# Performance work log

Measured on AMD Instinct MI355X. Metric: run time of the kernel, lower is better.

The kernel has to match this reference:

```python
import jax, jax.numpy as jnp
import numpy as np
import math

NUM_HEADS = 8
EPS = 1e-5
LEAKY_SLOPE = 0.01


def _attention(q, k, v, mask):
    # q:[S,64] k,v:[T,64] -> [S,64]; scale by sqrt(d) per source (q.shape[1])
    s = (q @ k.T) / math.sqrt(q.shape[1])
    if mask:
        S, T = s.shape
        tri = jnp.tril(jnp.ones((S, T), dtype=bool))
        s = jnp.where(tri, s, -jnp.inf)
    return jax.nn.softmax(s, axis=1) @ v


def _mha(q, k, v, w_o, mask):
    # all heads share the same (q,k,v) in the source, so cat over heads == tile
    head = _attention(q, k, v, mask)            # [S,64]
    concat = jnp.tile(head, (1, NUM_HEADS))     # [S,512]
    return concat @ w_o


def _layernorm(x, g, b):
    mu = jnp.mean(x, axis=-1, keepdims=True)
    var = jnp.var(x, axis=-1, keepdims=True)
    return (x - mu) * jax.lax.rsqrt(var + EPS) * g + b


def setup_inputs() -> dict:
    key = jax.random.key(0)
    ks = jax.random.split(key, 12)
    S, D, P, H = 8192, 512, 64, 2048
    sd = 1.0 / math.sqrt(D)
    return {
        "encoder_output": jax.random.normal(ks[0], (S, D), jnp.float32),
        "previous_stage_output": jax.random.normal(ks[1], (S, D), jnp.float32),
        "wq_m": jax.random.normal(ks[2], (D, P), jnp.float32) * sd,
        "wk_m": jax.random.normal(ks[3], (D, P), jnp.float32) * sd,
        "wv_m": jax.random.normal(ks[4], (D, P), jnp.float32) * sd,
        "wq_c": jax.random.normal(ks[5], (D, P), jnp.float32) * sd,
        "wk_c": jax.random.normal(ks[6], (D, P), jnp.float32) * sd,
        "wv_c": jax.random.normal(ks[7], (D, P), jnp.float32) * sd,
        "w_o": jax.random.normal(ks[8], (D, D), jnp.float32) * sd,
        "ln_g": jnp.ones((D,), jnp.float32),
        "ln_b": jnp.zeros((D,), jnp.float32),
        "w1": jax.random.normal(ks[9], (D, H), jnp.float32) * sd,
        "b1": jnp.zeros((H,), jnp.float32),
        "w2": jax.random.normal(ks[10], (H, D), jnp.float32) * (1.0 / math.sqrt(H)),
        "b2": jnp.zeros((D,), jnp.float32),
    }


def reference(encoder_output, previous_stage_output, wq_m, wk_m, wv_m,
              wq_c, wk_c, wv_c, w_o, ln_g, ln_b, w1, b1, w2, b2):
    prev = previous_stage_output
    # masked (causal) self-attention over previous decoder output
    masked_mh = _mha(prev @ wq_m, prev @ wk_m, prev @ wv_m, w_o, mask=True)
    # cross attention: q from masked output, k/v from encoder output
    mh = _mha(masked_mh @ wq_c, encoder_output @ wk_c, encoder_output @ wv_c,
              w_o, mask=False)
    x = _layernorm(mh + prev, ln_g, ln_b)
    h = x @ w1 + b1
    h = jnp.where(h >= 0, h, LEAKY_SLOPE * h)
    ffn = h @ w2 + b2
    out = _layernorm(ffn + x, ln_g, ln_b)
    return (encoder_output, out)
```

## Files before the change

kernel.cpp:

```cpp
#include <hip/hip_runtime.h>
#include <hip/hip_bf16.h>

typedef unsigned short u16;
typedef __attribute__((ext_vector_type(4))) float f32x4;
typedef __attribute__((ext_vector_type(8))) __bf16 bf16x8;
typedef __attribute__((ext_vector_type(8))) short short8;
typedef __attribute__((ext_vector_type(4))) short s16x4;

constexpr int SEQ = 8192;
constexpr int DM  = 512;
constexpr int HD  = 64;
constexpr int HFF = 2048;

__device__ __forceinline__ float b2f(u16 u){
  union { unsigned int i; float f; } v; v.i = ((unsigned int)u) << 16; return v.f;
}
__device__ __forceinline__ u16 f2b(float f){
  union { float f; unsigned int i; } v; v.f = f;
  unsigned int r = v.i + 0x7FFFu + ((v.i >> 16) & 1u);
  return (u16)(r >> 16);
}

__device__ __forceinline__ void gload16(const u16* g, u16* lds){
  __builtin_amdgcn_global_load_lds(
      (const __attribute__((address_space(1))) void*)g,
      (__attribute__((address_space(3))) void*)lds, 16, 0, 0);
}

__global__ __launch_bounds__(256) void cvt2_k(const float* __restrict__ enc,
                                              const float* __restrict__ prev,
                                              float* __restrict__ outf,
                                              u16* __restrict__ enc_b,
                                              u16* __restrict__ prev_b, long n8){
  long i = blockIdx.x * 256L + threadIdx.x;
  if(i >= n8) return;
  const float* in = blockIdx.y ? prev : enc;
  u16* ob = blockIdx.y ? prev_b : enc_b;
  f32x4 a = ((const f32x4*)in)[i*2];
  f32x4 b = ((const f32x4*)in)[i*2+1];
  if(!blockIdx.y){
    ((f32x4*)outf)[i*2]   = a;
    ((f32x4*)outf)[i*2+1] = b;
  }
  u16 ov[8];
  for(int j=0;j<4;j++){ ov[j] = f2b(a[j]); ov[4+j] = f2b(b[j]); }
  ((short8*)ob)[i] = *(short8*)ov;
}

__global__ __launch_bounds__(256) void prep_k(const float* __restrict__ p0,
                                              const float* __restrict__ p1,
                                              const float* __restrict__ p2,
                                              const float* __restrict__ p3,
                                              const float* __restrict__ p4,
                                              const float* __restrict__ p5,
                                              const float* __restrict__ w1,
                                              const float* __restrict__ w2,
                                              const float* __restrict__ wo,
                                              u16* __restrict__ out6,
                                              u16* __restrict__ w1_t,
                                              u16* __restrict__ w2_t,
                                              u16* __restrict__ wost,
                                              u16* __restrict__ wop){
  __shared__ u16 t[32][33];
  const int z = blockIdx.z;
  const int tx = threadIdx.x, ty = threadIdx.y;
  if(z < 6){
    if(blockIdx.x >= 2) return;
    const float* ins[6] = {p0,p1,p2,p3,p4,p5};
    const float* in = ins[z];
    u16* o = out6 + (long)z * 32768;
    int c0 = blockIdx.x*32, r0 = blockIdx.y*32;
    for(int i=0;i<4;i++)
      t[ty+i*8][tx] = f2b(in[(long)(r0+ty+i*8)*HD + c0+tx]);
    __syncthreads();
    for(int i=0;i<4;i++) o[(long)(c0+ty+i*8)*DM + r0+tx] = t[tx][ty+i*8];
  } else if(z == 6){
    int c0 = blockIdx.x*32, r0 = blockIdx.y*32;
    for(int i=0;i<4;i++)
      t[ty+i*8][tx] = f2b(w1[(long)(r0+ty+i*8)*HFF + c0+tx]);
    __syncthreads();
    for(int i=0;i<4;i++) w1_t[(long)(c0+ty+i*8)*DM + r0+tx] = t[tx][ty+i*8];
  } else if(z == 7){
    int c0 = blockIdx.y*32, r0 = blockIdx.x*32;
    for(int i=0;i<4;i++)
      t[ty+i*8][tx] = f2b(w2[(long)(r0+ty+i*8)*DM + c0+tx]);
    __syncthreads();
    for(int i=0;i<4;i++) w2_t[(long)(c0+ty+i*8)*HFF + r0+tx] = t[tx][ty+i*8];
  } else {
    int fb = blockIdx.y*64 + blockIdx.x;
    if(fb >= 128) return;
    int tid = fb*256 + ty*32 + tx;
    int n = tid >> 6, p = tid & 63;
    float s = 0.f;
    for(int h=0; h<8; h++) s += wo[(long)(h*64+p)*DM + n];
    u16 sv = f2b(s);
    wost[n*64 + p]  = sv;
    wop[p*DM + n]   = sv;
  }
}

__global__ __launch_bounds__(256) void vtrans2_k(const u16* __restrict__ v0,
                                                 u16* __restrict__ o0,
                                                 const u16* __restrict__ v1,
                                                 u16* __restrict__ o1){
  __shared__ u16 t[32][33];
  const u16* in = blockIdx.z ? v1 : v0;
  u16* o = blockIdx.z ? o1 : o0;
  int c0 = blockIdx.x*32, r0 = blockIdx.y*32;
  int tx = threadIdx.x, ty = threadIdx.y;
  for(int i=0;i<4;i++) t[ty+i*8][tx] = in[(long)(r0+ty+i*8)*HD + c0+tx];
  __syncthreads();
  for(int i=0;i<4;i++) o[(long)(c0+ty+i*8)*SEQ + r0+tx] = t[tx][ty+i*8];
}

template<bool WRITE_BF>
__global__ __launch_bounds__(256) void add_ln(const u16* __restrict__ Xa,
                                              const float* __restrict__ Xb,
                                              const float* __restrict__ G,
                                              const float* __restrict__ Bb,
                                              float* __restrict__ OutF,
                                              u16* __restrict__ OutB){
  int row  = blockIdx.x*4 + (threadIdx.x>>6);
  int lane = threadIdx.x & 63;
  short8 a8 = *(const short8*)&Xa[(long)row*DM + lane*8];
  f32x4 b0 = *(const f32x4*)&Xb[(long)row*DM + lane*8];
  f32x4 b1 = *(const f32x4*)&Xb[(long)row*DM + lane*8 + 4];
  float x[8]; float s=0.f, s2=0.f;
  for(int i=0;i<8;i++){
    float bv = (i<4) ? b0[i] : b1[i-4];
    x[i] = b2f((u16)a8[i]) + bv;
    s += x[i]; s2 += x[i]*x[i];
  }
  for(int o=1;o<64;o<<=1){ s += __shfl_xor(s,o); s2 += __shfl_xor(s2,o); }
  float mu  = s * (1.f/DM);
  float var = s2 * (1.f/DM) - mu*mu;
  float rstd = rsqrtf(var + 1e-5f);
  f32x4 g0 = *(const f32x4*)&G[lane*8];
  f32x4 g1 = *(const f32x4*)&G[lane*8+4];
  f32x4 p0 = *(const f32x4*)&Bb[lane*8];
  f32x4 p1 = *(const f32x4*)&Bb[lane*8+4];
  float of[8]; u16 ob[8];
  for(int i=0;i<8;i++){
    float gv = (i<4)?g0[i]:g1[i-4], bv2 = (i<4)?p0[i]:p1[i-4];
    float v = (x[i]-mu)*rstd*gv + bv2;
    of[i] = v; ob[i] = f2b(v);
  }
  *(f32x4*)&OutF[(long)row*DM + lane*8]     = *(f32x4*)&of[0];
  *(f32x4*)&OutF[(long)row*DM + lane*8 + 4] = *(f32x4*)&of[4];
  if constexpr (WRITE_BF)
    *(short8*)&OutB[(long)row*DM + lane*8] = *(short8*)ob;
}

template<int BM,int BN,int EPI,bool DBUF>
__global__ __launch_bounds__(256) void gemm2(const u16* __restrict__ A,
                                             const u16* __restrict__ Bt,
                                             u16* __restrict__ C,
                                             const float* __restrict__ bias,
                                             int N, int K, long sB, long sC){
  constexpr int WR=2, WC=2;
  constexpr int WM = BM/WR, WN = BN/WC;
  constexpr int MF = WM/16, NF = WN/16;
  constexpr int NB = DBUF ? 2 : 1;
  __shared__ u16 As[NB][BM*64];
  __shared__ u16 Bs[NB][BN*64];

  const int tid = threadIdx.x;
  const int wid = tid >> 6, lane = tid & 63;
  const int g = lane >> 4, lr = lane & 15;
  const int m0 = blockIdx.x * BM;
  const int n0 = blockIdx.y * BN;
  Bt += (long)blockIdx.z * sB;
  C  += (long)blockIdx.z * sC;
  const int wr = wid / WC, wc = wid % WC;

  f32x4 acc[MF][NF];
  for(int m=0;m<MF;m++) for(int n=0;n<NF;n++) acc[m][n] = (f32x4)0.f;

  auto stage = [&](const u16* src, int base_row, u16* lds, int rows, int k0){
    const int cpw = rows/32;
    for(int i=0;i<cpw;i++){
      int chunk = wid*cpw + i;
      int Lb = chunk*1024;
      int L  = Lb + lane*16;
      int row = L >> 7, cb = L & 127;
      int scb = cb ^ ((row&7)<<4);
      gload16(&src[(long)(base_row+row)*K + k0 + (scb>>1)], lds + (Lb>>1));
    }
  };
  auto compute = [&](const u16* As_, const u16* Bs_){
    for(int kc=0;kc<2;kc++){
      const int co = (kc*32 + g*8) ^ ((lr&7)<<3);
      bf16x8 af[MF], bfr[NF];
      for(int m=0;m<MF;m++) af[m]  = *(const bf16x8*)&As_[(wr*WM+m*16+lr)*64 + co];
      for(int n=0;n<NF;n++) bfr[n] = *(const bf16x8*)&Bs_[(wc*WN+n*16+lr)*64 + co];
      for(int m=0;m<MF;m++)
        for(int n=0;n<NF;n++)
          acc[m][n] = __builtin_amdgcn_mfma_f32_16x16x32_bf16(af[m], bfr[n], acc[m][n], 0,0,0);
    }
  };

  const int nk = K/64;
  if constexpr (DBUF){
    stage(A, m0, As[0], BM, 0);
    stage(Bt, n0, Bs[0], BN, 0);
    __syncthreads();
    int cur = 0;
    for(int t=0;t<nk;t++){
      if(t+1<nk){
        stage(A, m0, As[cur^1], BM, (t+1)*64);
        stage(Bt, n0, Bs[cur^1], BN, (t+1)*64);
      }
      compute(As[cur], Bs[cur]);
      __syncthreads();
      cur ^= 1;
    }
  } else {
    for(int t=0;t<nk;t++){
      stage(A, m0, As[0], BM, t*64);
      stage(Bt, n0, Bs[0], BN, t*64);
      __syncthreads();
      compute(As[0], Bs[0]);
      __syncthreads();
    }
  }
  for(int m=0;m<MF;m++){
    int row = m0 + wr*WM + m*16 + g*4;
    for(int n=0;n<NF;n++){
      int col = n0 + wc*WN + n*16 + lr;
      float bv = 0.f;
      if constexpr (EPI>=1) bv = bias[col];
      for(int j=0;j<4;j++){
        float v = acc[m][n][j] + bv;
        if constexpr (EPI==2) v = (v >= 0.f) ? v : 0.01f*v;
        C[(long)(row+j)*N + col] = f2b(v);
      }
    }
  }
}

template<bool CAUSAL>
__global__ __launch_bounds__(512) void attn_part_k(const u16* __restrict__ Q,
                                                   const u16* __restrict__ Km,
                                                   const u16* __restrict__ Vt,
                                                   u16* __restrict__ Op,
                                                   float* __restrict__ Ml){
  constexpr int LDK = 72;
  constexpr int NCH = 16;
  constexpr int CTI = 8;
  __shared__ u16 Ks[64*LDK];
  __shared__ u16 Vs[64*LDK];
  __shared__ u16 Ps[8*16*LDK];

  const int qb = blockIdx.x, ci = blockIdx.y;
  const int tdiag_b = 2*qb + 1 - ci*CTI;
  if(CAUSAL && tdiag_b < 0) return;

  const int tid = threadIdx.x, wid = tid>>6, lane = tid&63;
  const int g = lane>>4, lr = lane&15, r4 = g*4;
  const int qrow = qb*128 + wid*16;
  const int qb64 = qrow>>6;

  bf16x8 qf[2];
  for(int kc=0;kc<2;kc++){
    bf16x8 t = *(const bf16x8*)&Q[(long)(qrow + lr)*HD + kc*32 + g*8];
    for(int i=0;i<8;i++) t[i] = (__bf16)((float)t[i] * 0.1803368801f);
    qf[kc] = t;
  }

  f32x4 o[4]; for(int n=0;n<4;n++) o[n] = (f32x4)0.f;
  float lst = 0.f;

  const int tdiag_w = CAUSAL ? (qb64 - ci*CTI) : 0;
  const int tmax_w  = CAUSAL ? min(CTI, tdiag_w + 1) : CTI;
  const int tmax_b  = CAUSAL ? min(CTI, tdiag_b + 1) : CTI;
  const int kvbase  = ci*CTI*64;

  const int sr0 = tid>>3, sc0 = (tid&7)*8;
  short8 rK, rV;
  rK = *(const short8*)&Km[(long)(kvbase+sr0)*HD + sc0];
  rV = *(const short8*)&Vt[(long)sr0*SEQ + kvbase + sc0];

  for(int t=0; t<tmax_b; ++t){
    const int kv0 = kvbase + t*64;
    __syncthreads();
    *(short8*)&Ks[sr0*LDK + sc0] = rK;
    *(short8*)&Vs[sr0*LDK + sc0] = rV;
    __syncthreads();
    if(t+1 < tmax_b){
      const int kn = kv0 + 64;
      rK = *(const short8*)&Km[(long)(kn+sr0)*HD + sc0];
      rV = *(const short8*)&Vt[(long)sr0*SEQ + kn + sc0];
    }
    if(t < tmax_w){
      f32x4 s[4]; for(int n=0;n<4;n++) s[n] = (f32x4)0.f;
      for(int kc=0;kc<2;kc++){
        for(int n=0;n<4;n++){
          bf16x8 kf = *(const bf16x8*)&Ks[(n*16+lr)*LDK + kc*32 + g*8];
          s[n] = __builtin_amdgcn_mfma_f32_16x16x32_bf16(kf, qf[kc], s[n], 0,0,0);
        }
      }
      if(CAUSAL && t == tdiag_w){
        int row = qrow + lr;
        for(int n=0;n<4;n++)
          for(int j=0;j<4;j++)
            if(kv0 + n*16 + r4 + j > row) s[n][j] = -1e30f;
      }
      float rs = 0.f;
      for(int n=0;n<4;n++){
        u16 w[4];
        for(int j=0;j<4;j++){
          float p = exp2f(s[n][j]);
          rs += p;
          __bf16 pb = (__bf16)p;
          union { __bf16 b; u16 u; } cv; cv.b = pb;
          w[j] = cv.u;
        }
        *(s16x4*)&Ps[(wid*16 + lr)*LDK + n*16 + r4] = *(s16x4*)w;
      }
      rs += __shfl_xor(rs,16); rs += __shfl_xor(rs,32);
      lst += rs;
      for(int kc=0;kc<2;kc++){
        bf16x8 pf = *(const bf16x8*)&Ps[(wid*16 + lr)*LDK + kc*32 + g*8];
        for(int n=0;n<4;n++){
          bf16x8 vf = *(const bf16x8*)&Vs[(n*16+lr)*LDK + kc*32 + g*8];
          o[n] = __builtin_amdgcn_mfma_f32_16x16x32_bf16(pf, vf, o[n], 0,0,0);
        }
      }
    }
  }
  const long pr = (long)(qb64*NCH + ci)*64;
  const int ro = (wid&3)*16;
  for(int n=0;n<4;n++)
    for(int j=0;j<4;j++)
      Op[(pr + ro + r4 + j)*64 + n*16 + lr] = f2b(o[n][j]);
  if(lane < 16){
    Ml[(pr + ro + lr)*2]     = 0.f;
    Ml[(pr + ro + lr)*2 + 1] = lst;
  }
}

template<bool CAUSAL, int NCH>
__global__ __launch_bounds__(256) void attn_red_k(const u16* __restrict__ Op,
                                                  const float* __restrict__ Ml,
                                                  u16* __restrict__ O){
  constexpr int CTI = 128/NCH;
  int r = blockIdx.x*4 + (threadIdx.x>>6);
  int d = threadIdx.x & 63;
  int qb = r >> 6, rt = r & 63;
  int nch = CAUSAL ? (qb/CTI) + 1 : NCH;
  long base = (long)qb*NCH*64 + rt;
  float m = -1e30f;
  for(int i=0;i<nch;i++) m = fmaxf(m, Ml[(base + i*64)*2]);
  float L = 0.f, acc = 0.f;
  for(int i=0;i<nch;i++){
    float mi = Ml[(base + i*64)*2], li = Ml[(base + i*64)*2 + 1];
    float w = exp2f(mi - m);
    L   += li * w;
    acc += w * b2f(Op[(base + i*64)*64 + d]);
  }
  O[(long)r*HD + d] = f2b(acc / L);
}

extern "C" void kernel_launch(void* const* d_in, const int* in_sizes, int n_in,
                              void* d_out, int out_size, void* d_ws, size_t ws_size,
                              hipStream_t stream){
  const float* enc  = (const float*)d_in[0];
  const float* prev = (const float*)d_in[1];
  const float* wq_m = (const float*)d_in[2];
  const float* wk_m = (const float*)d_in[3];
  const float* wv_m = (const float*)d_in[4];
  const float* wq_c = (const float*)d_in[5];
  const float* wk_c = (const float*)d_in[6];
  const float* wv_c = (const float*)d_in[7];
  const float* w_o  = (const float*)d_in[8];
  const float* ln_g = (const float*)d_in[9];
  const float* ln_b = (const float*)d_in[10];
  const float* w1   = (const float*)d_in[11];
  const float* b1   = (const float*)d_in[12];
  const float* w2   = (const float*)d_in[13];
  const float* b2   = (const float*)d_in[14];
  float* out = (float*)d_out;
  u16* ws  = (u16*)d_ws;

  u16* wq_m_t = ws;
  u16* wq_c_t = wq_m_t + 3*32768;
  u16* wk_c_t = wq_m_t + 4*32768;
  u16* wost   = wq_m_t + 6*32768;
  u16* w1_t   = wost   + 32768;
  u16* w2_t   = w1_t   + 1048576;
  u16* enc_b  = w2_t   + 1048576;
  u16* prev_b = enc_b  + 4194304;
  u16* q_m    = prev_b + 4194304;
  u16* k_m    = q_m    + 524288;
  u16* v_m    = k_m    + 524288;
  u16* v_m_t  = v_m    + 524288;
  u16* head_m = v_m_t  + 524288;
  u16* k_c    = head_m + 524288;
  u16* v_c    = k_c    + 524288;
  u16* v_c_t  = v_c    + 524288;
  u16* q_c    = v_c_t  + 524288;
  u16* head_c = q_c    + 524288;
  u16* mmh    = head_c + 524288;
  u16* mh     = mmh    + 4194304;
  u16* xb     = mh     + 4194304;
  float* xf   = (float*)(xb + 4194304);
  u16* wop    = (u16*)(xf + 4194304);
  u16* weffT  = wop + 32768;
  u16* hbuf   = enc_b;
  u16* ffn    = mh;
  u16* Op     = mmh;
  float* Ml   = (float*)(Op + (long)128*16*64*64);

  dim3 b256(256), b512(512), tb(32,8);

  cvt2_k<<<dim3(2048,2), b256, 0, stream>>>(enc, prev, out, enc_b, prev_b, (long)SEQ*DM/8);

  prep_k<<<dim3(64,16,9), tb, 0, stream>>>(wq_m, wk_m, wv_m, wq_c, wk_c, wv_c,
                                           w1, w2, w_o, wq_m_t, w1_t, w2_t, wost, wop);

  gemm2<64,64,0,true><<<dim3(1,1,1), b256, 0, stream>>>(wq_c_t, wop, weffT, nullptr, 64, 512, 0, 0);

  gemm2<64,64,0,true><<<dim3(SEQ/64,1,3), b256, 0, stream>>>(prev_b, wq_m_t, q_m, nullptr, HD, DM, 32768, 524288);
  gemm2<64,64,0,true><<<dim3(SEQ/64,1,2), b256, 0, stream>>>(enc_b,  wk_c_t, k_c, nullptr, HD, DM, 32768, 524288);
  vtrans2_k<<<dim3(2,256,2), tb, 0, stream>>>(v_m, v_m_t, v_c, v_c_t);

  attn_part_k<true><<<dim3(SEQ/128, 16), b512, 0, stream>>>(q_m, k_m, v_m_t, Op, Ml);
  attn_red_k<true,16><<<dim3(SEQ/4), b256, 0, stream>>>(Op, Ml, head_m);

  gemm2<64,64,0,false><<<dim3(SEQ/64,1,1), b256, 0, stream>>>(head_m, weffT, q_c, nullptr, HD, HD, 0, 0);

  attn_part_k<false><<<dim3(SEQ/128, 16), b512, 0, stream>>>(q_c, k_c, v_c_t, Op, Ml);
  attn_red_k<false,16><<<dim3(SEQ/4), b256, 0, stream>>>(Op, Ml, head_c);
  gemm2<64,128,0,false><<<dim3(SEQ/64,4,1), b256, 0, stream>>>(head_c, wost, mh, nullptr, DM, HD, 0, 0);

  add_ln<true><<<dim3(SEQ/4), b256, 0, stream>>>(mh, prev, ln_g, ln_b, xf, xb);

  gemm2<64,128,2,false><<<dim3(SEQ/64,HFF/128,1), b256, 0, stream>>>(xb, w1_t, hbuf, b1, HFF, DM, 0, 0);
  gemm2<64,128,1,true><<<dim3(SEQ/64,4,1),        b256, 0, stream>>>(hbuf, w2_t, ffn, b2, DM, HFF, 0, 0);

  add_ln<false><<<dim3(SEQ/4), b256, 0, stream>>>(ffn, xf, ln_g, ln_b, out + (long)SEQ*DM, nullptr);
}
```

Measured before the change: 206.4 us.

## Merge Q/K/V projection launches, add MFMA priority hints, retune FFN2 template

Replaces the two projection GEMM launches (three on the previous-stage output, two on the encoder output) with a single dedicated kernel over a z-grid of five. The kernel uses swizzled LDS, double buffering and direct global-to-LDS loads. It also wraps the MFMA sections of the attention kernel in s_setprio raises so matrix work gets issue priority over other waves. It flips the boolean template flag of the second FFN GEMM, presumably switching its load path variant. Together these aim to cut launch overhead and improve scheduling, at the risk of regressing the FFN GEMM if the other variant is slower.

```diff
diff --git a/kernel.cpp b/kernel.cpp
--- a/kernel.cpp
+++ b/kernel.cpp
@@ -238,6 +238,74 @@
   }
 }
 
+__global__ __launch_bounds__(256) void gemm_proj(const u16* __restrict__ A0,
+                                                 const u16* __restrict__ A1,
+                                                 const u16* __restrict__ Wt,
+                                                 u16* __restrict__ C0,
+                                                 u16* __restrict__ C1){
+  constexpr int BM=64, BN=64;
+  __shared__ u16 As[2][BM*64];
+  __shared__ u16 Bs[2][BN*64];
+
+  const int z = blockIdx.z;
+  const u16* A  = (z<3) ? A0 : A1;
+  const u16* Bt = Wt + (long)((z<3)? z : z+1) * 32768;
+  u16* C        = (z<3) ? (C0 + (long)z*524288) : (C1 + (long)(z-3)*524288);
+
+  const int tid = threadIdx.x;
+  const int wid = tid >> 6, lane = tid & 63;
+  const int g = lane >> 4, lr = lane & 15;
+  const int m0 = blockIdx.x * BM;
+  const int wr = wid >> 1, wc = wid & 1;
+
+  f32x4 acc[2][2];
+  for(int m=0;m<2;m++) for(int n=0;n<2;n++) acc[m][n] = (f32x4)0.f;
+
+  auto stage = [&](const u16* src, int base_row, u16* lds, int k0){
+    for(int i=0;i<2;i++){
+      int chunk = wid*2 + i;
+      int Lb = chunk*1024;
+      int L  = Lb + lane*16;
+      int row = L >> 7, cb = L & 127;
+      int scb = cb ^ ((row&7)<<4);
+      gload16(&src[(long)(base_row+row)*DM + k0 + (scb>>1)], lds + (Lb>>1));
+    }
+  };
+  auto compute = [&](const u16* As_, const u16* Bs_){
+    for(int kc=0;kc<2;kc++){
+      const int co = (kc*32 + g*8) ^ ((lr&7)<<3);
+      bf16x8 af[2], bfr[2];
+      for(int m=0;m<2;m++) af[m]  = *(const bf16x8*)&As_[(wr*32+m*16+lr)*64 + co];
+      for(int n=0;n<2;n++) bfr[n] = *(const bf16x8*)&Bs_[(wc*32+n*16+lr)*64 + co];
+      for(int m=0;m<2;m++)
+        for(int n=0;n<2;n++)
+          acc[m][n] = __builtin_amdgcn_mfma_f32_16x16x32_bf16(af[m], bfr[n], acc[m][n], 0,0,0);
+    }
+  };
+
+  stage(A, m0, As[0], 0);
+  stage(Bt, 0, Bs[0], 0);
+  __syncthreads();
+  int cur = 0;
+  for(int t=0;t<8;t++){
+    if(t+1<8){
+      stage(A, m0, As[cur^1], (t+1)*64);
+      stage(Bt, 0, Bs[cur^1], (t+1)*64);
+    }
+    compute(As[cur], Bs[cur]);
+    __syncthreads();
+    cur ^= 1;
+  }
+  for(int m=0;m<2;m++){
+    int row = m0 + wr*32 + m*16 + g*4;
+    for(int n=0;n<2;n++){
+      int col = wc*32 + n*16 + lr;
+      for(int j=0;j<4;j++)
+        C[(long)(row+j)*HD + col] = f2b(acc[m][n][j]);
+    }
+  }
+}
+
 template<bool CAUSAL>
 __global__ __launch_bounds__(512) void attn_part_k(const u16* __restrict__ Q,
                                                    const u16* __restrict__ Km,
@@ -293,12 +361,14 @@
     }
     if(t < tmax_w){
       f32x4 s[4]; for(int n=0;n<4;n++) s[n] = (f32x4)0.f;
+      __builtin_amdgcn_s_setprio(1);
       for(int kc=0;kc<2;kc++){
         for(int n=0;n<4;n++){
           bf16x8 kf = *(const bf16x8*)&Ks[(n*16+lr)*LDK + kc*32 + g*8];
           s[n] = __builtin_amdgcn_mfma_f32_16x16x32_bf16(kf, qf[kc], s[n], 0,0,0);
         }
       }
+      __builtin_amdgcn_s_setprio(0);
       if(CAUSAL && t == tdiag_w){
         int row = qrow + lr;
         for(int n=0;n<4;n++)
@@ -319,6 +389,7 @@
       }
       rs += __shfl_xor(rs,16); rs += __shfl_xor(rs,32);
       lst += rs;
+      __builtin_amdgcn_s_setprio(1);
       for(int kc=0;kc<2;kc++){
         bf16x8 pf = *(const bf16x8*)&Ps[(wid*16 + lr)*LDK + kc*32 + g*8];
         for(int n=0;n<4;n++){
@@ -326,6 +397,7 @@
           o[n] = __builtin_amdgcn_mfma_f32_16x16x32_bf16(pf, vf, o[n], 0,0,0);
         }
       }
+      __builtin_amdgcn_s_setprio(0);
     }
   }
   const long pr = (long)(qb64*NCH + ci)*64;
@@ -384,7 +456,6 @@
 
   u16* wq_m_t = ws;
   u16* wq_c_t = wq_m_t + 3*32768;
-  u16* wk_c_t = wq_m_t + 4*32768;
   u16* wost   = wq_m_t + 6*32768;
   u16* w1_t   = wost   + 32768;
   u16* w2_t   = w1_t   + 1048576;
@@ -420,8 +491,7 @@
 
   gemm2<64,64,0,true><<<dim3(1,1,1), b256, 0, stream>>>(wq_c_t, wop, weffT, nullptr, 64, 512, 0, 0);
 
-  gemm2<64,64,0,true><<<dim3(SEQ/64,1,3), b256, 0, stream>>>(prev_b, wq_m_t, q_m, nullptr, HD, DM, 32768, 524288);
-  gemm2<64,64,0,true><<<dim3(SEQ/64,1,2), b256, 0, stream>>>(enc_b,  wk_c_t, k_c, nullptr, HD, DM, 32768, 524288);
+  gemm_proj<<<dim3(SEQ/64,1,5), b256, 0, stream>>>(prev_b, enc_b, wq_m_t, q_m, k_c);
   vtrans2_k<<<dim3(2,256,2), tb, 0, stream>>>(v_m, v_m_t, v_c, v_c_t);
 
   attn_part_k<true><<<dim3(SEQ/128, 16), b512, 0, stream>>>(q_m, k_m, v_m_t, Op, Ml);
@@ -436,7 +506,7 @@
   add_ln<true><<<dim3(SEQ/4), b256, 0, stream>>>(mh, prev, ln_g, ln_b, xf, xb);
 
   gemm2<64,128,2,false><<<dim3(SEQ/64,HFF/128,1), b256, 0, stream>>>(xb, w1_t, hbuf, b1, HFF, DM, 0, 0);
-  gemm2<64,128,1,true><<<dim3(SEQ/64,4,1),        b256, 0, stream>>>(hbuf, w2_t, ffn, b2, DM, HFF, 0, 0);
+  gemm2<64,128,1,false><<<dim3(SEQ/64,4,1),       b256, 0, stream>>>(hbuf, w2_t, ffn, b2, DM, HFF, 0, 0);
 
   add_ln<false><<<dim3(SEQ/4), b256, 0, stream>>>(ffn, xf, ln_g, ln_b, out + (long)SEQ*DM, nullptr);
 }
```

Measured after the change: 204.0 us, median of 2. About the same (-1.1%).
